# Kernel tuning notes

Measured on AMD Instinct MI355X. Metric: run time of the kernel, lower is better.

## Reference

```python
import jax, jax.numpy as jnp
import numpy as np

B, S, D, H = 4, 2048, 1024, 16
HD = D // H

def setup_inputs() -> dict:
    key = jax.random.key(0)
    ks = jax.random.split(key, 4)
    return {
        "x": jax.random.normal(ks[0], (B, S, D), dtype=jnp.float32),
        "W_attn": jax.random.normal(ks[1], (H, HD, HD), dtype=jnp.float32) * 0.02,
        "W_in": jax.random.normal(ks[2], (D, D), dtype=jnp.float32) * 0.02,
        "b_in": jnp.zeros((D,), dtype=jnp.float32),
        "W_out": jax.random.normal(ks[3], (D, D), dtype=jnp.float32) * 0.02,
        "b_out": jnp.zeros((D,), dtype=jnp.float32),
    }

def reference(x, W_attn, W_in, b_in, W_out, b_out):
    bsz, seq_len, d = x.shape
    h = x @ W_in + b_in                                   # [B,S,D] in_project
    h = h.reshape(bsz, seq_len, H, HD).transpose(0, 2, 1, 3)  # [B,H,S,hd]
    q = jnp.einsum('bhsd,hde->bhse', h, W_attn)           # x @ attn_weight
    scores = jnp.einsum('bhse,bhte->bhst', q, h) / HD     # [B,H,S,S]
    w = jax.nn.softmax(scores, axis=-1)                   # attn_output_weights_1
    # dropout omitted (eval/deterministic mode)
    out = jnp.einsum('bhst,bhtd->bhsd', w, h)             # [B,H,S,hd]
    out = out.transpose(0, 2, 1, 3).reshape(bsz, seq_len, d)
    out = out @ W_out + b_out                             # out_project
    return out, w
```

## Files before the change

### kernel.cpp

```cpp
#include <hip/hip_runtime.h>
#include <hip/hip_bf16.h>
#include <stdint.h>

#define DEV __device__ __forceinline__

constexpr int B_ = 4, S_ = 2048, D_ = 1024, H_ = 16, HD_ = 64;
constexpr int BH_ = B_ * H_;
constexpr int BS_ = B_ * S_;

typedef __attribute__((ext_vector_type(8))) short bf16x8;
typedef __attribute__((ext_vector_type(4))) float f32x4;

constexpr float SCL = 0.022542110013890053f;

DEV float fast_exp2(float x) { return __builtin_amdgcn_exp2f(x); }

DEV uint16_t f2bf(float f) {
    union { float f; uint32_t u; } v; v.f = f;
    return (uint16_t)((v.u + 0x7fffu + ((v.u >> 16) & 1u)) >> 16);
}

DEV uint16_t f2bf_fast(float f) {
    __hip_bfloat16 h = __float2bfloat16(f);
    uint16_t u; __builtin_memcpy(&u, &h, 2);
    return u;
}

DEV f32x4 mfma16(bf16x8 a, bf16x8 b, f32x4 c) {
    return __builtin_amdgcn_mfma_f32_16x16x32_bf16(a, b, c, 0, 0, 0);
}

__global__ __launch_bounds__(256) void k_prep(
    const float* __restrict__ Win, const float* __restrict__ Wout,
    const float* __restrict__ Wa, const float* __restrict__ x,
    uint16_t* __restrict__ WtIn, uint16_t* __restrict__ WtOut,
    uint16_t* __restrict__ WtA, uint16_t* __restrict__ xb) {
    int stride = gridDim.x * blockDim.x;
    int idx = blockIdx.x * blockDim.x + threadIdx.x;
    for (int i = idx; i < BS_ * D_ / 4; i += stride) {
        float4 v = reinterpret_cast<const float4*>(x)[i];
        ushort4 o;
        o.x = f2bf(v.x); o.y = f2bf(v.y); o.z = f2bf(v.z); o.w = f2bf(v.w);
        reinterpret_cast<ushort4*>(xb)[i] = o;
    }
    for (int i = idx; i < D_ * D_; i += stride) {
        int n = i / D_, k = i % D_;
        WtIn[i]  = f2bf(Win[(size_t)k * D_ + n]);
        WtOut[i] = f2bf(Wout[(size_t)k * D_ + n]);
    }
    for (int i = idx; i < H_ * HD_ * HD_; i += stride) {
        int h = i / (HD_ * HD_);
        int r = i % (HD_ * HD_);
        int e = r / HD_, d = r % HD_;
        WtA[i] = f2bf(Wa[((size_t)h * HD_ + d) * HD_ + e]);
    }
}

__global__ __launch_bounds__(256) void k_gemm_in(
    const uint16_t* __restrict__ xb, const uint16_t* __restrict__ WtIn,
    const float* __restrict__ b_in, uint16_t* __restrict__ hb) {
    const int wave = threadIdx.x >> 6, lane = threadIdx.x & 63;
    const int lhi = lane >> 4, llo = lane & 15;
    const int L = blockIdx.x, xcd = L & 7, slot = L >> 3;
    const int col0 = ((xcd << 1) | (slot & 1)) * 64;
    const int row0 = (slot >> 1) * 64 + wave * 16;

    f32x4 acc[4] = {};
    const uint16_t* xrow = xb + (size_t)(row0 + llo) * D_;
    for (int kc = 0; kc < D_ / 32; ++kc) {
        const int k0 = kc * 32 + lhi * 8;
        bf16x8 a = *reinterpret_cast<const bf16x8*>(xrow + k0);
#pragma unroll
        for (int nt = 0; nt < 4; ++nt) {
            const uint16_t* bp = WtIn + (size_t)(col0 + nt * 16 + llo) * D_ + k0;
            bf16x8 b = *reinterpret_cast<const bf16x8*>(bp);
            acc[nt] = mfma16(a, b, acc[nt]);
        }
    }
#pragma unroll
    for (int nt = 0; nt < 4; ++nt) {
        const int c = col0 + nt * 16 + llo;
        const float bias = b_in[c];
        const int bhcol = c >> 6, d = c & 63;
#pragma unroll
        for (int r = 0; r < 4; ++r) {
            const int m = row0 + lhi * 4 + r;
            const int b_ = m >> 11, s = m & 2047;
            hb[((size_t)(b_ * H_ + bhcol) * S_ + s) * HD_ + d] = f2bf(acc[nt][r] + bias);
        }
    }
}

__global__ __launch_bounds__(256) void k_transpose(
    const uint16_t* __restrict__ hb, uint16_t* __restrict__ hbT) {
    __shared__ uint16_t tile[64][72];
    const int st = blockIdx.x, bh = blockIdx.y;
    const int s0 = st * 64;
    const int t = threadIdx.x;
    {
        const int r = t >> 2, c0 = (t & 3) * 16;
        const uint16_t* src = hb + ((size_t)bh * S_ + s0 + r) * HD_ + c0;
        *reinterpret_cast<bf16x8*>(&tile[r][c0])     = *reinterpret_cast<const bf16x8*>(src);
        *reinterpret_cast<bf16x8*>(&tile[r][c0 + 8]) = *reinterpret_cast<const bf16x8*>(src + 8);
    }
    __syncthreads();
    {
        const int d = t >> 2, c0 = (t & 3) * 16;
        uint16_t tmp[16];
#pragma unroll
        for (int j = 0; j < 16; ++j) tmp[j] = tile[c0 + j][d];
        uint16_t* dst = hbT + ((size_t)bh * HD_ + d) * S_ + s0 + c0;
        *reinterpret_cast<bf16x8*>(dst)     = *reinterpret_cast<const bf16x8*>(tmp);
        *reinterpret_cast<bf16x8*>(dst + 8) = *reinterpret_cast<const bf16x8*>(tmp + 8);
    }
}

__global__ __launch_bounds__(256) void k_gemm_q(
    const uint16_t* __restrict__ hb, const uint16_t* __restrict__ WtA,
    uint16_t* __restrict__ qb) {
    const int wave = threadIdx.x >> 6, lane = threadIdx.x & 63;
    const int lhi = lane >> 4, llo = lane & 15;
    const int bh = blockIdx.y;
    const int h = bh & (H_ - 1);
    const int row0 = blockIdx.x * 64 + wave * 16;

    const uint16_t* hrow = hb + ((size_t)bh * S_ + row0 + llo) * HD_;
    f32x4 acc[4] = {};
#pragma unroll
    for (int kc = 0; kc < 2; ++kc) {
        const int k0 = kc * 32 + lhi * 8;
        bf16x8 a = *reinterpret_cast<const bf16x8*>(hrow + k0);
#pragma unroll
        for (int nt = 0; nt < 4; ++nt) {
            bf16x8 b = *reinterpret_cast<const bf16x8*>(
                WtA + ((size_t)h * HD_ + nt * 16 + llo) * HD_ + k0);
            acc[nt] = mfma16(a, b, acc[nt]);
        }
    }
#pragma unroll
    for (int nt = 0; nt < 4; ++nt) {
        const int e = nt * 16 + llo;
#pragma unroll
        for (int r = 0; r < 4; ++r) {
            const int s = row0 + lhi * 4 + r;
            qb[((size_t)bh * S_ + s) * HD_ + e] = f2bf(acc[nt][r]);
        }
    }
}

__global__ __launch_bounds__(256) void k_attn_fused(
    const uint16_t* __restrict__ qb, const uint16_t* __restrict__ hb,
    const uint16_t* __restrict__ hbT, float* __restrict__ w_out,
    uint16_t* __restrict__ pvb) {
    __shared__ uint16_t wb[4][32 * 72];

    const int tid = threadIdx.x;
    const int wave = tid >> 6, lane = tid & 63;
    const int lhi = lane >> 4, llo = lane & 15;

    const int L = blockIdx.x;
    const int xcd = L & 7, slot = L >> 3;
    const int bh = (xcd << 3) | (slot >> 4);
    const int row0 = (slot & 15) * 128 + wave * 32;

    const uint16_t* hbase  = hb  + (size_t)bh * S_ * HD_;
    const uint16_t* hTbase = hbT + (size_t)bh * HD_ * S_;

    bf16x8 a[2][2];
#pragma unroll
    for (int g = 0; g < 2; ++g) {
        const uint16_t* qrow = qb + ((size_t)bh * S_ + row0 + g * 16 + llo) * HD_;
        a[g][0] = *reinterpret_cast<const bf16x8*>(qrow + lhi * 8);
        a[g][1] = *reinterpret_cast<const bf16x8*>(qrow + 32 + lhi * 8);
    }

    float sume[2][4] = {};
    for (int tch = 0; tch < 32; ++tch) {
        const int t0 = tch * 64;
        bf16x8 b0[4], b1[4];
#pragma unroll
        for (int ct = 0; ct < 4; ++ct) {
            const uint16_t* hrow = hbase + (size_t)(t0 + ct * 16 + llo) * HD_ + lhi * 8;
            b0[ct] = *reinterpret_cast<const bf16x8*>(hrow);
            b1[ct] = *reinterpret_cast<const bf16x8*>(hrow + 32);
        }
#pragma unroll
        for (int g = 0; g < 2; ++g) {
#pragma unroll
            for (int ct = 0; ct < 4; ++ct) {
                f32x4 acc = {};
                acc = mfma16(a[g][0], b0[ct], acc);
                acc = mfma16(a[g][1], b1[ct], acc);
#pragma unroll
                for (int r = 0; r < 4; ++r) sume[g][r] += fast_exp2(acc[r] * SCL);
            }
        }
    }
    float inv[2][4];
#pragma unroll
    for (int g = 0; g < 2; ++g) {
#pragma unroll
        for (int r = 0; r < 4; ++r) {
            float v = sume[g][r];
            v += __shfl_xor(v, 1); v += __shfl_xor(v, 2);
            v += __shfl_xor(v, 4); v += __shfl_xor(v, 8);
            inv[g][r] = 1.0f / v;
        }
    }

    f32x4 pv[2][4] = {};
    uint16_t* mywb = &wb[wave][0];
    float* wrow_base = w_out + ((size_t)bh * S_ + row0) * S_;

    for (int tch = 0; tch < 32; ++tch) {
        const int t0 = tch * 64;
        bf16x8 b0[4], b1[4];
#pragma unroll
        for (int ct = 0; ct < 4; ++ct) {
            const uint16_t* hrow = hbase + (size_t)(t0 + ct * 16 + llo) * HD_ + lhi * 8;
            b0[ct] = *reinterpret_cast<const bf16x8*>(hrow);
            b1[ct] = *reinterpret_cast<const bf16x8*>(hrow + 32);
        }
#pragma unroll
        for (int g = 0; g < 2; ++g) {
#pragma unroll
            for (int ct = 0; ct < 4; ++ct) {
                f32x4 acc = {};
                acc = mfma16(a[g][0], b0[ct], acc);
                acc = mfma16(a[g][1], b1[ct], acc);
#pragma unroll
                for (int r = 0; r < 4; ++r) {
                    const int rr = g * 16 + lhi * 4 + r;
                    const int cc = ct * 16 + llo;
                    float wv = fast_exp2(acc[r] * SCL) * inv[g][r];
                    __builtin_nontemporal_store(
                        wv, wrow_base + (size_t)rr * S_ + t0 + cc);
                    mywb[rr * 72 + cc] = f2bf_fast(wv);
                }
            }
        }
#pragma unroll
        for (int g = 0; g < 2; ++g) {
#pragma unroll
            for (int kk = 0; kk < 2; ++kk) {
                bf16x8 aw = *reinterpret_cast<const bf16x8*>(
                    &mywb[(g * 16 + llo) * 72 + kk * 32 + lhi * 8]);
#pragma unroll
                for (int dt = 0; dt < 4; ++dt) {
                    bf16x8 b = *reinterpret_cast<const bf16x8*>(
                        hTbase + (size_t)(dt * 16 + llo) * S_ + t0 + kk * 32 + lhi * 8);
                    pv[g][dt] = mfma16(aw, b, pv[g][dt]);
                }
            }
        }
    }

    const int b_ = bh >> 4, h = bh & (H_ - 1);
#pragma unroll
    for (int g = 0; g < 2; ++g) {
#pragma unroll
        for (int dt = 0; dt < 4; ++dt) {
            const int d = dt * 16 + llo;
#pragma unroll
            for (int r = 0; r < 4; ++r) {
                const int s = row0 + g * 16 + lhi * 4 + r;
                pvb[((size_t)(b_ * S_ + s)) * D_ + h * HD_ + d] = f2bf(pv[g][dt][r]);
            }
        }
    }
}

__global__ __launch_bounds__(256) void k_gemm_out(
    const uint16_t* __restrict__ pvb, const uint16_t* __restrict__ WtOut,
    const float* __restrict__ b_out, float* __restrict__ out) {
    const int wave = threadIdx.x >> 6, lane = threadIdx.x & 63;
    const int lhi = lane >> 4, llo = lane & 15;
    const int L = blockIdx.x, xcd = L & 7, slot = L >> 3;
    const int col0 = ((xcd << 1) | (slot & 1)) * 64;
    const int row0 = (slot >> 1) * 64 + wave * 16;

    const uint16_t* prow = pvb + (size_t)(row0 + llo) * D_;
    f32x4 acc[4] = {};
    for (int kc = 0; kc < D_ / 32; ++kc) {
        const int k0 = kc * 32 + lhi * 8;
        bf16x8 a = *reinterpret_cast<const bf16x8*>(prow + k0);
#pragma unroll
        for (int nt = 0; nt < 4; ++nt) {
            bf16x8 b = *reinterpret_cast<const bf16x8*>(
                WtOut + (size_t)(col0 + nt * 16 + llo) * D_ + k0);
            acc[nt] = mfma16(a, b, acc[nt]);
        }
    }
#pragma unroll
    for (int nt = 0; nt < 4; ++nt) {
        const int c = col0 + nt * 16 + llo;
        const float bias = b_out[c];
#pragma unroll
        for (int r = 0; r < 4; ++r) {
            out[(size_t)(row0 + lhi * 4 + r) * D_ + c] = acc[nt][r] + bias;
        }
    }
}

extern "C" void kernel_launch(void* const* d_in, const int* in_sizes, int n_in,
                              void* d_out, int out_size, void* d_ws, size_t ws_size,
                              hipStream_t stream) {
    const float* x      = (const float*)d_in[0];
    const float* W_attn = (const float*)d_in[1];
    const float* W_in   = (const float*)d_in[2];
    const float* b_in   = (const float*)d_in[3];
    const float* W_out  = (const float*)d_in[4];
    const float* b_out  = (const float*)d_in[5];

    float* out   = (float*)d_out;
    float* w_out = out + (size_t)BS_ * D_;

    uint8_t* ws = (uint8_t*)d_ws;
    auto carve = [&](size_t elems) {
        uint16_t* p = (uint16_t*)ws;
        ws += ((elems * sizeof(uint16_t) + 255) / 256) * 256;
        return p;
    };
    uint16_t* WtIn  = carve((size_t)D_ * D_);
    uint16_t* WtOut = carve((size_t)D_ * D_);
    uint16_t* WtA   = carve((size_t)H_ * HD_ * HD_);
    uint16_t* xb    = carve((size_t)BS_ * D_);
    uint16_t* hb    = carve((size_t)BH_ * S_ * HD_);
    uint16_t* hbT   = carve((size_t)BH_ * HD_ * S_);
    uint16_t* qb    = carve((size_t)BH_ * S_ * HD_);
    uint16_t* pvb   = xb;

    hipLaunchKernelGGL(k_prep, dim3(2048), dim3(256), 0, stream,
                       W_in, W_out, W_attn, x, WtIn, WtOut, WtA, xb);
    hipLaunchKernelGGL(k_gemm_in, dim3(2048), dim3(256), 0, stream,
                       xb, WtIn, b_in, hb);
    hipLaunchKernelGGL(k_transpose, dim3(32, 64), dim3(256), 0, stream, hb, hbT);
    hipLaunchKernelGGL(k_gemm_q, dim3(32, 64), dim3(256), 0, stream, hb, WtA, qb);
    hipLaunchKernelGGL(k_attn_fused, dim3(1024), dim3(256), 0, stream,
                       qb, hb, hbT, w_out, pvb);
    hipLaunchKernelGGL(k_gemm_out, dim3(2048), dim3(256), 0, stream,
                       pvb, WtOut, b_out, out);
}
```

Before: 756.7 us.

## Fuse in-projection, transpose and q-GEMM; double-buffer h loads in attention

```diff
diff --git a/kernel.cpp b/kernel.cpp
--- a/kernel.cpp
+++ b/kernel.cpp
@@ -56,95 +56,82 @@
     }
 }
 
-__global__ __launch_bounds__(256) void k_gemm_in(
+__global__ __launch_bounds__(256) void k_proj(
     const uint16_t* __restrict__ xb, const uint16_t* __restrict__ WtIn,
-    const float* __restrict__ b_in, uint16_t* __restrict__ hb) {
-    const int wave = threadIdx.x >> 6, lane = threadIdx.x & 63;
+    const float* __restrict__ b_in, const uint16_t* __restrict__ WtA,
+    uint16_t* __restrict__ hb, uint16_t* __restrict__ hbT,
+    uint16_t* __restrict__ qb) {
+    __shared__ uint16_t ht[64][72];
+    const int tid = threadIdx.x;
+    const int wave = tid >> 6, lane = tid & 63;
     const int lhi = lane >> 4, llo = lane & 15;
     const int L = blockIdx.x, xcd = L & 7, slot = L >> 3;
     const int col0 = ((xcd << 1) | (slot & 1)) * 64;
-    const int row0 = (slot >> 1) * 64 + wave * 16;
+    const int row0 = (slot >> 1) * 64;
+    const int wrow = wave * 16;
 
     f32x4 acc[4] = {};
-    const uint16_t* xrow = xb + (size_t)(row0 + llo) * D_;
+    const uint16_t* xrow = xb + (size_t)(row0 + wrow + llo) * D_;
     for (int kc = 0; kc < D_ / 32; ++kc) {
         const int k0 = kc * 32 + lhi * 8;
         bf16x8 a = *reinterpret_cast<const bf16x8*>(xrow + k0);
 #pragma unroll
         for (int nt = 0; nt < 4; ++nt) {
-            const uint16_t* bp = WtIn + (size_t)(col0 + nt * 16 + llo) * D_ + k0;
-            bf16x8 b = *reinterpret_cast<const bf16x8*>(bp);
+            bf16x8 b = *reinterpret_cast<const bf16x8*>(
+                WtIn + (size_t)(col0 + nt * 16 + llo) * D_ + k0);
             acc[nt] = mfma16(a, b, acc[nt]);
         }
     }
+
+    const int head = (col0 >> 6) & (H_ - 1);
+    const int bh = ((row0 >> 11) << 4) | head;
+    const int s0 = row0 & (S_ - 1);
+
 #pragma unroll
     for (int nt = 0; nt < 4; ++nt) {
         const int c = col0 + nt * 16 + llo;
         const float bias = b_in[c];
-        const int bhcol = c >> 6, d = c & 63;
+        const int d = c & 63;
 #pragma unroll
         for (int r = 0; r < 4; ++r) {
-            const int m = row0 + lhi * 4 + r;
-            const int b_ = m >> 11, s = m & 2047;
-            hb[((size_t)(b_ * H_ + bhcol) * S_ + s) * HD_ + d] = f2bf(acc[nt][r] + bias);
-        }
-    }
-}
-
-__global__ __launch_bounds__(256) void k_transpose(
-    const uint16_t* __restrict__ hb, uint16_t* __restrict__ hbT) {
-    __shared__ uint16_t tile[64][72];
-    const int st = blockIdx.x, bh = blockIdx.y;
-    const int s0 = st * 64;
-    const int t = threadIdx.x;
+            const int rr = wrow + lhi * 4 + r;
+            const uint16_t u = f2bf(acc[nt][r] + bias);
+            hb[((size_t)bh * S_ + s0 + rr) * HD_ + d] = u;
+            ht[rr][d] = u;
+        }
+    }
+    __syncthreads();
+
+    f32x4 qa[4] = {};
+#pragma unroll
+    for (int kc = 0; kc < 2; ++kc) {
+        const int k0 = kc * 32 + lhi * 8;
+        bf16x8 a = *reinterpret_cast<const bf16x8*>(&ht[wrow + llo][k0]);
+#pragma unroll
+        for (int nt = 0; nt < 4; ++nt) {
+            bf16x8 b = *reinterpret_cast<const bf16x8*>(
+                WtA + ((size_t)head * HD_ + nt * 16 + llo) * HD_ + k0);
+            qa[nt] = mfma16(a, b, qa[nt]);
+        }
+    }
+#pragma unroll
+    for (int nt = 0; nt < 4; ++nt) {
+        const int e = nt * 16 + llo;
+#pragma unroll
+        for (int r = 0; r < 4; ++r) {
+            const int s = s0 + wrow + lhi * 4 + r;
+            qb[((size_t)bh * S_ + s) * HD_ + e] = f2bf(qa[nt][r]);
+        }
+    }
+
     {
-        const int r = t >> 2, c0 = (t & 3) * 16;
-        const uint16_t* src = hb + ((size_t)bh * S_ + s0 + r) * HD_ + c0;
-        *reinterpret_cast<bf16x8*>(&tile[r][c0])     = *reinterpret_cast<const bf16x8*>(src);
-        *reinterpret_cast<bf16x8*>(&tile[r][c0 + 8]) = *reinterpret_cast<const bf16x8*>(src + 8);
-    }
-    __syncthreads();
-    {
-        const int d = t >> 2, c0 = (t & 3) * 16;
+        const int d = tid >> 2, c0 = (tid & 3) * 16;
         uint16_t tmp[16];
 #pragma unroll
-        for (int j = 0; j < 16; ++j) tmp[j] = tile[c0 + j][d];
+        for (int j = 0; j < 16; ++j) tmp[j] = ht[c0 + j][d];
         uint16_t* dst = hbT + ((size_t)bh * HD_ + d) * S_ + s0 + c0;
         *reinterpret_cast<bf16x8*>(dst)     = *reinterpret_cast<const bf16x8*>(tmp);
         *reinterpret_cast<bf16x8*>(dst + 8) = *reinterpret_cast<const bf16x8*>(tmp + 8);
-    }
-}
-
-__global__ __launch_bounds__(256) void k_gemm_q(
-    const uint16_t* __restrict__ hb, const uint16_t* __restrict__ WtA,
-    uint16_t* __restrict__ qb) {
-    const int wave = threadIdx.x >> 6, lane = threadIdx.x & 63;
-    const int lhi = lane >> 4, llo = lane & 15;
-    const int bh = blockIdx.y;
-    const int h = bh & (H_ - 1);
-    const int row0 = blockIdx.x * 64 + wave * 16;
-
-    const uint16_t* hrow = hb + ((size_t)bh * S_ + row0 + llo) * HD_;
-    f32x4 acc[4] = {};
-#pragma unroll
-    for (int kc = 0; kc < 2; ++kc) {
-        const int k0 = kc * 32 + lhi * 8;
-        bf16x8 a = *reinterpret_cast<const bf16x8*>(hrow + k0);
-#pragma unroll
-        for (int nt = 0; nt < 4; ++nt) {
-            bf16x8 b = *reinterpret_cast<const bf16x8*>(
-                WtA + ((size_t)h * HD_ + nt * 16 + llo) * HD_ + k0);
-            acc[nt] = mfma16(a, b, acc[nt]);
-        }
-    }
-#pragma unroll
-    for (int nt = 0; nt < 4; ++nt) {
-        const int e = nt * 16 + llo;
-#pragma unroll
-        for (int r = 0; r < 4; ++r) {
-            const int s = row0 + lhi * 4 + r;
-            qb[((size_t)bh * S_ + s) * HD_ + e] = f2bf(acc[nt][r]);
-        }
     }
 }
 
@@ -174,16 +161,19 @@
         a[g][1] = *reinterpret_cast<const bf16x8*>(qrow + 32 + lhi * 8);
     }
 
-    float sume[2][4] = {};
-    for (int tch = 0; tch < 32; ++tch) {
+    auto loadh = [&](int tch, bf16x8 (&b0)[4], bf16x8 (&b1)[4]) {
         const int t0 = tch * 64;
-        bf16x8 b0[4], b1[4];
 #pragma unroll
         for (int ct = 0; ct < 4; ++ct) {
-            const uint16_t* hrow = hbase + (size_t)(t0 + ct * 16 + llo) * HD_ + lhi * 8;
+            const uint16_t* hrow =
+                hbase + (size_t)(t0 + ct * 16 + llo) * HD_ + lhi * 8;
             b0[ct] = *reinterpret_cast<const bf16x8*>(hrow);
             b1[ct] = *reinterpret_cast<const bf16x8*>(hrow + 32);
         }
+    };
+
+    float sume[2][4] = {};
+    auto p1 = [&](bf16x8 (&b0)[4], bf16x8 (&b1)[4]) {
 #pragma unroll
         for (int g = 0; g < 2; ++g) {
 #pragma unroll
@@ -194,6 +184,16 @@
 #pragma unroll
                 for (int r = 0; r < 4; ++r) sume[g][r] += fast_exp2(acc[r] * SCL);
             }
+        }
+    };
+    {
+        bf16x8 A0[4], A1[4], B0[4], B1[4];
+        loadh(0, A0, A1);
+        for (int tch = 0; tch < 32; tch += 2) {
+            loadh(tch + 1, B0, B1);
+            p1(A0, A1);
+            if (tch + 2 < 32) loadh(tch + 2, A0, A1);
+            p1(B0, B1);
         }
     }
     float inv[2][4];
@@ -212,15 +212,8 @@
     uint16_t* mywb = &wb[wave][0];
     float* wrow_base = w_out + ((size_t)bh * S_ + row0) * S_;
 
-    for (int tch = 0; tch < 32; ++tch) {
+    auto p2 = [&](int tch, bf16x8 (&b0)[4], bf16x8 (&b1)[4]) {
         const int t0 = tch * 64;
-        bf16x8 b0[4], b1[4];
-#pragma unroll
-        for (int ct = 0; ct < 4; ++ct) {
-            const uint16_t* hrow = hbase + (size_t)(t0 + ct * 16 + llo) * HD_ + lhi * 8;
-            b0[ct] = *reinterpret_cast<const bf16x8*>(hrow);
-            b1[ct] = *reinterpret_cast<const bf16x8*>(hrow + 32);
-        }
 #pragma unroll
         for (int g = 0; g < 2; ++g) {
 #pragma unroll
@@ -252,6 +245,16 @@
                     pv[g][dt] = mfma16(aw, b, pv[g][dt]);
                 }
             }
+        }
+    };
+    {
+        bf16x8 A0[4], A1[4], B0[4], B1[4];
+        loadh(0, A0, A1);
+        for (int tch = 0; tch < 32; tch += 2) {
+            loadh(tch + 1, B0, B1);
+            p2(tch, A0, A1);
+            if (tch + 2 < 32) loadh(tch + 2, A0, A1);
+            p2(tch + 1, B0, B1);
         }
     }
 
@@ -332,10 +335,8 @@
 
     hipLaunchKernelGGL(k_prep, dim3(2048), dim3(256), 0, stream,
                        W_in, W_out, W_attn, x, WtIn, WtOut, WtA, xb);
-    hipLaunchKernelGGL(k_gemm_in, dim3(2048), dim3(256), 0, stream,
-                       xb, WtIn, b_in, hb);
-    hipLaunchKernelGGL(k_transpose, dim3(32, 64), dim3(256), 0, stream, hb, hbT);
-    hipLaunchKernelGGL(k_gemm_q, dim3(32, 64), dim3(256), 0, stream, hb, WtA, qb);
+    hipLaunchKernelGGL(k_proj, dim3(2048), dim3(256), 0, stream,
+                       xb, WtIn, b_in, WtA, hb, hbT, qb);
     hipLaunchKernelGGL(k_attn_fused, dim3(1024), dim3(256), 0, stream,
                        qb, hb, hbT, w_out, pvb);
     hipLaunchKernelGGL(k_gemm_out, dim3(2048), dim3(256), 0, stream,
```

Result: faster. 712.2 us (-5.9%).
